# Kernel tuning notes

Measured on AMD Instinct MI355X. Metric: run time of the kernel, lower is better.

## Reference

```python
import jax, jax.numpy as jnp
import numpy as np

PI = 3.141592653589793
B, N, NUM_CLASSES = 512, 128, 10
Q_LAYERS = 3

# state layout: [B, Xc, Xa, Yc, Ya, F]  (Xc/Yc = condition (pooled) dims, Xa/Ya = active dims, F = feature dim = 2)

def _qft2d(s):
    # unitary QFT over both active spatial axes
    s = jnp.fft.fft(s, axis=2, norm="ortho")
    return jnp.fft.fft(s, axis=4, norm="ortho")

def _iqft2d(s):
    s = jnp.fft.ifft(s, axis=2, norm="ortho")
    return jnp.fft.ifft(s, axis=4, norm="ortho")

def _pool(s):
    # move the most significant active qubit of each axis into the condition register
    b, xc, xa, yc, ya, f = s.shape
    s = s.reshape(b, xc, 2, xa // 2, yc, 2, ya // 2, f)
    return s.reshape(b, xc * 2, xa // 2, yc * 2, ya // 2, f)

def _multiplex(s, coeffs):
    # coeffs: [cx, cy, Xa, Ya, 3] Pauli coefficients; applies exp(-i a.sigma) on the
    # feature qubit per Fourier mode, conditioned on the most recently pooled bit per axis.
    cx, cy = coeffs.shape[0], coeffs.shape[1]
    b, xc, xa, yc, ya, f = s.shape
    s = s.reshape(b, xc // cx, cx, xa, yc // cy, cy, ya, f)
    c = jnp.transpose(coeffs, (0, 2, 1, 3, 4))[None, None, :, :, None]  # [1,1,cx,Xa,1,cy,Ya,3]
    ax, ay, az = c[..., 0], c[..., 1], c[..., 2]
    r = jnp.sqrt(ax * ax + ay * ay + az * az + 1e-20)
    cr = jnp.cos(r)
    sn = jnp.sin(r) / r
    u00 = (cr - 1j * az * sn).astype(s.dtype)
    u01 = ((-1j * ax - ay) * sn).astype(s.dtype)
    u10 = ((-1j * ax + ay) * sn).astype(s.dtype)
    u11 = (cr + 1j * az * sn).astype(s.dtype)
    p0, p1 = s[..., 0], s[..., 1]
    out = jnp.stack([u00 * p0 + u01 * p1, u10 * p0 + u11 * p1], axis=-1)
    return out.reshape(b, xc, xa, yc, ya, f)

def _forward(images, mux0, mux1, mux2, W, b_):
    # FRQI encoder: theta in brightness_range (0, pi); feature qubit cos/sin amplitudes
    theta = PI * images
    amp = jnp.stack([jnp.cos(theta * 0.5), jnp.sin(theta * 0.5)], axis=-1) / images.shape[-1]
    state = amp.astype(jnp.complex64)[:, None, :, None, :, :]  # [B,1,N,1,N,2]
    muxes = (mux0, mux1, mux2)
    state = _qft2d(state)
    for li, coeffs in enumerate(muxes):
        state = _multiplex(state, coeffs)
        if li < len(muxes) - 1:
            # reduced Fourier junction == IQFT -> pool -> QFT
            state = _qft2d(_pool(_iqft2d(state)))
        else:
            state = _iqft2d(state)
    # marginal measurement over condition registers -> [B, Xa, Ya, F]
    prob = jnp.sum(jnp.abs(state) ** 2, axis=(1, 3))
    flat = prob.reshape(prob.shape[0], -1)
    return flat @ W.T + b_

def setup_inputs() -> dict:
    key = jax.random.key(0)
    ks = jax.random.split(key, 6)
    scale = 2.0 * PI
    images = jax.random.uniform(ks[0], (B, N, N), dtype=jnp.float32)
    mux0 = jax.random.uniform(ks[1], (1, 1, 128, 128, 3), dtype=jnp.float32) * scale
    mux1 = jax.random.uniform(ks[2], (2, 2, 64, 64, 3), dtype=jnp.float32) * scale
    mux2 = jax.random.uniform(ks[3], (2, 2, 32, 32, 3), dtype=jnp.float32) * scale
    W = jax.random.normal(ks[4], (NUM_CLASSES, 32 * 32 * 2), dtype=jnp.float32) * 0.02
    b_ = jnp.zeros((NUM_CLASSES,), dtype=jnp.float32)
    return {"images": images, "mux0": mux0, "mux1": mux1, "mux2": mux2, "W": W, "b_": b_}

def reference(images, mux0, mux1, mux2, W, b_):
    return _forward(images, mux0, mux1, mux2, W, b_)
```

## Files before the change

kernel.cpp:

```cpp
#include <hip/hip_runtime.h>
#include <math.h>


#define PI_F 3.14159265358979323846f
#define P_ 128

__device__ __forceinline__ float2 cmul(float2 a, float2 b) {
    return make_float2(a.x * b.x - a.y * b.y, a.x * b.y + a.y * b.x);
}
__device__ __forceinline__ float2 cadd(float2 a, float2 b) {
    return make_float2(a.x + b.x, a.y + b.y);
}
__device__ __forceinline__ float2 scl(float2 a, float s) {
    return make_float2(a.x * s, a.y * s);
}
__device__ __forceinline__ void bfly_dif(float2& u, float2& v, float2 w) {
    float tx = u.x - v.x, ty = u.y - v.y;
    u.x += v.x; u.y += v.y;
    v.x = tx * w.x - ty * w.y;
    v.y = tx * w.y + ty * w.x;
}
__device__ __forceinline__ void bfly_dif1(float2& u, float2& v) {
    float tx = u.x - v.x, ty = u.y - v.y;
    u.x += v.x; u.y += v.y;
    v.x = tx; v.y = ty;
}
__device__ __forceinline__ void bfly_dit(float2& u, float2& v, float2 w) {
    float tx = v.x * w.x + v.y * w.y, ty = v.y * w.x - v.x * w.y;
    v.x = u.x - tx; v.y = u.y - ty;
    u.x += tx; u.y += ty;
}
__device__ __forceinline__ void bfly_dit1(float2& u, float2& v) {
    float tx = v.x, ty = v.y;
    v.x = u.x - tx; v.y = u.y - ty;
    u.x += tx; u.y += ty;
}

constexpr int clog2(int v) { return v <= 1 ? 0 : 1 + clog2(v >> 1); }

__device__ __forceinline__ int pf(int L, int idx) {
    int m = ((idx & 32) ? 13 : 0) ^ ((idx & 64) ? 22 : 0);
    return L * P_ + (idx ^ m);
}

template <int N, int S>
__device__ __forceinline__ void oidx(int j, int i[4], int& o) {
    constexpr int TPS = N / 4;
    constexpr int LT = clog2(TPS);
    int s = j >> LT;
    int jj = j & (TPS - 1);
    o = jj & (S - 1);
    int base = s * N + ((jj & ~(S - 1)) << 2) + o;
    i[0] = base; i[1] = base + S; i[2] = base + 2 * S; i[3] = base + 3 * S;
}

template <int S>
__device__ __forceinline__ void dif_pair(float2 r[4], int o, const float2* tw) {
    bfly_dif(r[0], r[2], tw[o * (32 / S)]);
    bfly_dif(r[1], r[3], tw[(o + S) * (32 / S)]);
    float2 wc = tw[o * (64 / S)];
    bfly_dif(r[0], r[1], wc);
    bfly_dif(r[2], r[3], wc);
}
template <int S>
__device__ __forceinline__ void dit_pair(float2 r[4], int o, const float2* tw) {
    float2 wc = tw[o * (64 / S)];
    bfly_dit(r[0], r[1], wc);
    bfly_dit(r[2], r[3], wc);
    bfly_dit(r[0], r[2], tw[o * (32 / S)]);
    bfly_dit(r[1], r[3], tw[(o + S) * (32 / S)]);
}

__device__ __forceinline__ void stf(float* bx, float* by, int a, float2 v) {
    bx[a] = v.x; by[a] = v.y;
}
__device__ __forceinline__ float2 ldf(const float* bx, const float* by, int a) {
    return make_float2(bx[a], by[a]);
}

template <int NW, int SW, int NR, int SR>
__device__ __forceinline__ int xchg(float* bx, float* by, int L, int j,
                                    float2 r[4]) {
    int iw[4], ow;
    oidx<NW, SW>(j, iw, ow);
    stf(bx, by, pf(L, iw[0]), r[0]); stf(bx, by, pf(L, iw[1]), r[1]);
    stf(bx, by, pf(L, iw[2]), r[2]); stf(bx, by, pf(L, iw[3]), r[3]);
    __builtin_amdgcn_wave_barrier();
    int ir[4], orr;
    oidx<NR, SR>(j, ir, orr);
    r[0] = ldf(bx, by, pf(L, ir[0])); r[1] = ldf(bx, by, pf(L, ir[1]));
    r[2] = ldf(bx, by, pf(L, ir[2])); r[3] = ldf(bx, by, pf(L, ir[3]));
    __builtin_amdgcn_wave_barrier();
    return orr;
}

__device__ __forceinline__ void tw_init(float2* tw, int tid) {
    if (tid < 64) {
        float s, c;
        sincosf(-(2.0f * PI_F / 128.0f) * (float)tid, &s, &c);
        tw[tid] = make_float2(c, s);
    }
}

__global__ __launch_bounds__(256) void k0_prep(const float* __restrict__ mux0,
                                               const float* __restrict__ mux1,
                                               const float* __restrict__ mux2,
                                               float2* __restrict__ U0,
                                               float2* __restrict__ U1,
                                               float2* __restrict__ U2) {
    int t = blockIdx.x * 256 + threadIdx.x;
    const float* src;
    float2* dst;
    if (t < 16384) {
        int xb = t >> 7, yb = t & 127;
        int rx = __brev((unsigned)xb) >> 25;
        int ry = __brev((unsigned)yb) >> 25;
        src = mux0 + ((size_t)rx * 128 + ry) * 3;
        dst = U0 + (size_t)t * 4;
    } else if (t < 32768) {
        int u = t - 16384;
        int yam = u & 63, xam = (u >> 6) & 63, cy = (u >> 12) & 1, cx = (u >> 13) & 1;
        int rx = __brev((unsigned)xam) >> 26;
        int ry = __brev((unsigned)yam) >> 26;
        src = mux1 + ((size_t)(((cx * 2 + cy) * 64 + rx) * 64 + ry)) * 3;
        dst = U1 + (size_t)u * 4;
    } else if (t < 36864) {
        int u = t - 32768;
        int yam = u & 31, xam = (u >> 5) & 31, cy = (u >> 10) & 1, cx = (u >> 11) & 1;
        int rx = __brev((unsigned)xam) >> 27;
        int ry = __brev((unsigned)yam) >> 27;
        src = mux2 + ((size_t)(((cx * 2 + cy) * 32 + rx) * 32 + ry)) * 3;
        dst = U2 + (size_t)u * 4;
    } else {
        return;
    }
    float ax = src[0], ay = src[1], az = src[2];
    float r = sqrtf(ax * ax + ay * ay + az * az + 1e-20f);
    float cr = cosf(r);
    float snr = sinf(r) / r;
    dst[0] = make_float2(cr, -az * snr);
    dst[1] = make_float2(-ay * snr, -ax * snr);
    dst[2] = make_float2(ay * snr, -ax * snr);
    dst[3] = make_float2(cr, az * snr);
}

__global__ __launch_bounds__(256) void k1_encode(const float* __restrict__ img,
                                                 float2* __restrict__ S) {
    __shared__ float Ax[8 * P_], Ay[8 * P_], Bx[8 * P_], By[8 * P_];
    __shared__ float2 tw[64];
    int tid = threadIdx.x;
    tw_init(tw, tid);
    int b = blockIdx.x >> 5;
    int X0 = (blockIdx.x & 31) * 4;
    int L = tid >> 5, j = tid & 31;
    int row = L >> 1, f = L & 1;
    const float* ip = img + ((size_t)(b * 128) + X0 + row) * 128;
    float2 r[4];
#pragma unroll
    for (int q = 0; q < 4; ++q) {
        float v = ip[j + 32 * q];
        float s, c;
        sincosf(0.5f * PI_F * v, &s, &c);
        float a = f ? s : c;
        r[q] = make_float2(a * (1.0f / 128.0f), 0.0f);
    }
    __syncthreads();
    dif_pair<32>(r, j, tw);
    int o = xchg<128, 32, 128, 8>(Ax, Ay, L, j, r);
    dif_pair<8>(r, o, tw);
    o = xchg<128, 8, 128, 2>(Bx, By, L, j, r);
    dif_pair<2>(r, o, tw);
    o = xchg<128, 2, 128, 1>(Ax, Ay, L, j, r);
    bfly_dif1(r[0], r[1]); bfly_dif1(r[2], r[3]);
    float2* op = S + ((size_t)((b * 128 + X0 + row) * 2 + f)) * 128 + 4 * j;
    float4* gp = (float4*)op;
    gp[0] = make_float4(r[0].x, r[0].y, r[1].x, r[1].y);
    gp[1] = make_float4(r[2].x, r[2].y, r[3].x, r[3].y);
}

__global__ __launch_bounds__(256) void k2_col0(float2* __restrict__ S,
                                               const float2* __restrict__ U0) {
    __shared__ float Ax[8 * P_], Ay[8 * P_], Bx[8 * P_], By[8 * P_];
    __shared__ float2 tw[64];
    int tid = threadIdx.x;
    tw_init(tw, tid);
    int b = blockIdx.x >> 5;
    int s_ = blockIdx.x & 31;
    int Y0 = (((s_ & 7) << 2) | (s_ >> 3)) * 4;
    {
        int X = tid & 127, f = tid >> 7;
        const float4* gp = (const float4*)(S + ((size_t)((b * 128 + X) * 2 + f)) * 128 + Y0);
        float4 v0 = gp[0], v1 = gp[1];
        stf(Ax, Ay, pf(f * 4 + 0, X), make_float2(v0.x, v0.y));
        stf(Ax, Ay, pf(f * 4 + 1, X), make_float2(v0.z, v0.w));
        stf(Ax, Ay, pf(f * 4 + 2, X), make_float2(v1.x, v1.y));
        stf(Ax, Ay, pf(f * 4 + 3, X), make_float2(v1.z, v1.w));
    }
    __syncthreads();
    int L = tid >> 5, j = tid & 31;
    float2 r[4];
    int o;
    {
        int ir[4];
        oidx<128, 32>(j, ir, o);
        r[0] = ldf(Ax, Ay, pf(L, ir[0])); r[1] = ldf(Ax, Ay, pf(L, ir[1]));
        r[2] = ldf(Ax, Ay, pf(L, ir[2])); r[3] = ldf(Ax, Ay, pf(L, ir[3]));
    }
    dif_pair<32>(r, o, tw);
    o = xchg<128, 32, 128, 8>(Bx, By, L, j, r);
    dif_pair<8>(r, o, tw);
    o = xchg<128, 8, 128, 2>(Ax, Ay, L, j, r);
    dif_pair<2>(r, o, tw);
    {
        int iw[4], ow;
        oidx<128, 2>(j, iw, ow);
        stf(Bx, By, pf(L, iw[0]), r[0]); stf(Bx, By, pf(L, iw[1]), r[1]);
        stf(Bx, By, pf(L, iw[2]), r[2]); stf(Bx, By, pf(L, iw[3]), r[3]);
    }
    __syncthreads();
    int yl = tid >> 6, m2 = (tid & 63) * 2;
    r[0] = ldf(Bx, By, pf(yl, m2));     r[1] = ldf(Bx, By, pf(4 + yl, m2));
    r[2] = ldf(Bx, By, pf(yl, m2 + 1)); r[3] = ldf(Bx, By, pf(4 + yl, m2 + 1));
    bfly_dif1(r[0], r[2]); bfly_dif1(r[1], r[3]);
    {
        const float2* U = U0 + ((size_t)m2 * 128 + (Y0 + yl)) * 4;
        float2 p0 = r[0], p1 = r[1];
        r[0] = cadd(cmul(U[0], p0), cmul(U[1], p1));
        r[1] = cadd(cmul(U[2], p0), cmul(U[3], p1));
        U = U0 + ((size_t)(m2 + 1) * 128 + (Y0 + yl)) * 4;
        p0 = r[2]; p1 = r[3];
        r[2] = cadd(cmul(U[0], p0), cmul(U[1], p1));
        r[3] = cadd(cmul(U[2], p0), cmul(U[3], p1));
    }
    bfly_dit1(r[0], r[2]); bfly_dit1(r[1], r[3]);
    stf(Ax, Ay, pf(yl, m2), r[0]);     stf(Ax, Ay, pf(4 + yl, m2), r[1]);
    stf(Ax, Ay, pf(yl, m2 + 1), r[2]); stf(Ax, Ay, pf(4 + yl, m2 + 1), r[3]);
    __syncthreads();
    {
        int ir[4];
        oidx<128, 2>(j, ir, o);
        r[0] = ldf(Ax, Ay, pf(L, ir[0])); r[1] = ldf(Ax, Ay, pf(L, ir[1]));
        r[2] = ldf(Ax, Ay, pf(L, ir[2])); r[3] = ldf(Ax, Ay, pf(L, ir[3]));
    }
    dit_pair<2>(r, o, tw);
    o = xchg<128, 2, 128, 8>(Bx, By, L, j, r);
    dit_pair<8>(r, o, tw);
    o = xchg<128, 8, 128, 32>(Ax, Ay, L, j, r);
    dit_pair<32>(r, o, tw);
    {
        float2 w = tw[2 * o];
        bfly_dif(r[0], r[1], w); bfly_dif(r[2], r[3], w);
    }
    o = xchg<128, 32, 64, 8>(Bx, By, L, j, r);
    dif_pair<8>(r, o, tw);
    o = xchg<64, 8, 64, 2>(Ax, Ay, L, j, r);
    dif_pair<2>(r, o, tw);
    o = xchg<64, 2, 64, 1>(Bx, By, L, j, r);
    bfly_dif1(r[0], r[1]); bfly_dif1(r[2], r[3]);
    {
        int iw[4], ow;
        oidx<64, 1>(j, iw, ow);
        const float sc = 1.0f / 128.0f;
        stf(Ax, Ay, pf(L, iw[0]), scl(r[0], sc));
        stf(Ax, Ay, pf(L, iw[1]), scl(r[1], sc));
        stf(Ax, Ay, pf(L, iw[2]), scl(r[2], sc));
        stf(Ax, Ay, pf(L, iw[3]), scl(r[3], sc));
    }
    __syncthreads();
    {
        int X = tid & 127, f = tid >> 7;
        float2 e0 = ldf(Ax, Ay, pf(f * 4 + 0, X));
        float2 e1 = ldf(Ax, Ay, pf(f * 4 + 1, X));
        float2 e2 = ldf(Ax, Ay, pf(f * 4 + 2, X));
        float2 e3 = ldf(Ax, Ay, pf(f * 4 + 3, X));
        float4* gp = (float4*)(S + ((size_t)((b * 128 + X) * 2 + f)) * 128 + Y0);
        gp[0] = make_float4(e0.x, e0.y, e1.x, e1.y);
        gp[1] = make_float4(e2.x, e2.y, e3.x, e3.y);
    }
}

__global__ __launch_bounds__(256) void k3_row1(float2* __restrict__ S,
                                               const float2* __restrict__ U1) {
    __shared__ float Ax[8 * P_], Ay[8 * P_], Bx[8 * P_], By[8 * P_];
    __shared__ float2 tw[64];
    int tid = threadIdx.x;
    tw_init(tw, tid);
    int b = blockIdx.x >> 5;
    int X0 = (blockIdx.x & 31) * 4;
    int L = tid >> 5, j = tid & 31;
    int row = L >> 1, f = L & 1;
    float2* gl = S + ((size_t)((b * 128 + X0 + row) * 2 + f)) * 128;
    float2 r[4];
    {
        const float4* gp = (const float4*)(gl + 4 * j);
        float4 v0 = gp[0], v1 = gp[1];
        r[0] = make_float2(v0.x, v0.y); r[1] = make_float2(v0.z, v0.w);
        r[2] = make_float2(v1.x, v1.y); r[3] = make_float2(v1.z, v1.w);
    }
    __syncthreads();
    dit_pair<1>(r, 0, tw);
    int o = xchg<128, 1, 128, 4>(Ax, Ay, L, j, r);
    dit_pair<4>(r, o, tw);
    o = xchg<128, 4, 128, 16>(Bx, By, L, j, r);
    dit_pair<16>(r, o, tw);
    o = xchg<128, 16, 128, 32>(Ax, Ay, L, j, r);
    bfly_dit(r[0], r[2], tw[o]);
    bfly_dit(r[1], r[3], tw[o + 32]);
    {
        float2 w = tw[2 * o];
        bfly_dif(r[0], r[1], w); bfly_dif(r[2], r[3], w);
    }
    o = xchg<128, 32, 64, 8>(Bx, By, L, j, r);
    dif_pair<8>(r, o, tw);
    o = xchg<64, 8, 64, 2>(Ax, Ay, L, j, r);
    dif_pair<2>(r, o, tw);
    {
        int iw[4], ow;
        oidx<64, 2>(j, iw, ow);
        stf(Bx, By, pf(L, iw[0]), r[0]); stf(Bx, By, pf(L, iw[1]), r[1]);
        stf(Bx, By, pf(L, iw[2]), r[2]); stf(Bx, By, pf(L, iw[3]), r[3]);
    }
    __syncthreads();
    int row2 = tid >> 6, m2 = (tid & 63) * 2;
    r[0] = ldf(Bx, By, pf(row2 * 2, m2));
    r[1] = ldf(Bx, By, pf(row2 * 2 + 1, m2));
    r[2] = ldf(Bx, By, pf(row2 * 2, m2 + 1));
    r[3] = ldf(Bx, By, pf(row2 * 2 + 1, m2 + 1));
    bfly_dif1(r[0], r[2]); bfly_dif1(r[1], r[3]);
    {
        int X = X0 + row2;
        int cx = X >> 6, xam = X & 63;
        int cy0 = m2 >> 6, yam0 = m2 & 63;
        const float2* U =
            U1 + ((size_t)((((cx << 1) | cy0) << 6 | xam) << 6 | yam0)) * 4;
        float2 p0 = r[0], p1 = r[1];
        r[0] = cadd(cmul(U[0], p0), cmul(U[1], p1));
        r[1] = cadd(cmul(U[2], p0), cmul(U[3], p1));
        int cy1 = (m2 + 1) >> 6, yam1 = (m2 + 1) & 63;
        U = U1 + ((size_t)((((cx << 1) | cy1) << 6 | xam) << 6 | yam1)) * 4;
        p0 = r[2]; p1 = r[3];
        r[2] = cadd(cmul(U[0], p0), cmul(U[1], p1));
        r[3] = cadd(cmul(U[2], p0), cmul(U[3], p1));
    }
    bfly_dit1(r[0], r[2]); bfly_dit1(r[1], r[3]);
    stf(Ax, Ay, pf(row2 * 2, m2), r[0]);
    stf(Ax, Ay, pf(row2 * 2 + 1, m2), r[1]);
    stf(Ax, Ay, pf(row2 * 2, m2 + 1), r[2]);
    stf(Ax, Ay, pf(row2 * 2 + 1, m2 + 1), r[3]);
    __syncthreads();
    {
        int ir[4];
        oidx<64, 2>(j, ir, o);
        r[0] = ldf(Ax, Ay, pf(L, ir[0])); r[1] = ldf(Ax, Ay, pf(L, ir[1]));
        r[2] = ldf(Ax, Ay, pf(L, ir[2])); r[3] = ldf(Ax, Ay, pf(L, ir[3]));
    }
    dit_pair<2>(r, o, tw);
    o = xchg<64, 2, 64, 8>(Bx, By, L, j, r);
    dit_pair<8>(r, o, tw);
    o = xchg<64, 8, 64, 16>(Ax, Ay, L, j, r);
    bfly_dit(r[0], r[2], tw[2 * o]);
    bfly_dit(r[1], r[3], tw[2 * o + 32]);
    {
        float2 w = tw[4 * o];
        bfly_dif(r[0], r[1], w); bfly_dif(r[2], r[3], w);
    }
    o = xchg<64, 16, 32, 4>(Bx, By, L, j, r);
    dif_pair<4>(r, o, tw);
    o = xchg<32, 4, 32, 1>(Ax, Ay, L, j, r);
    dif_pair<1>(r, 0, tw);
    {
        int iw[4], ow;
        oidx<32, 1>(j, iw, ow);
        const float sc = 1.0f / 8192.0f;
        float4* gp = (float4*)(gl + iw[0]);
        gp[0] = make_float4(r[0].x * sc, r[0].y * sc, r[1].x * sc, r[1].y * sc);
        gp[1] = make_float4(r[2].x * sc, r[2].y * sc, r[3].x * sc, r[3].y * sc);
    }
}

__global__ __launch_bounds__(256) void k4_col2(float2* __restrict__ S,
                                               const float2* __restrict__ U2) {
    __shared__ float Ax[8 * P_], Ay[8 * P_], Bx[8 * P_], By[8 * P_];
    __shared__ float2 tw[64];
    int tid = threadIdx.x;
    tw_init(tw, tid);
    int b = blockIdx.x >> 5;
    int s_ = blockIdx.x & 31;
    int Y0 = (((s_ & 7) << 2) | (s_ >> 3)) * 4;
    {
        int X = tid & 127, f = tid >> 7;
        const float4* gp = (const float4*)(S + ((size_t)((b * 128 + X) * 2 + f)) * 128 + Y0);
        float4 v0 = gp[0], v1 = gp[1];
        stf(Ax, Ay, pf(f * 4 + 0, X), make_float2(v0.x, v0.y));
        stf(Ax, Ay, pf(f * 4 + 1, X), make_float2(v0.z, v0.w));
        stf(Ax, Ay, pf(f * 4 + 2, X), make_float2(v1.x, v1.y));
        stf(Ax, Ay, pf(f * 4 + 3, X), make_float2(v1.z, v1.w));
    }
    __syncthreads();
    int L = tid >> 5, j = tid & 31;
    float2 r[4];
    int o;
    {
        int ir[4];
        oidx<64, 1>(j, ir, o);
        r[0] = ldf(Ax, Ay, pf(L, ir[0])); r[1] = ldf(Ax, Ay, pf(L, ir[1]));
        r[2] = ldf(Ax, Ay, pf(L, ir[2])); r[3] = ldf(Ax, Ay, pf(L, ir[3]));
    }
    dit_pair<1>(r, 0, tw);
    o = xchg<64, 1, 64, 4>(Bx, By, L, j, r);
    dit_pair<4>(r, o, tw);
    o = xchg<64, 4, 64, 16>(Ax, Ay, L, j, r);
    dit_pair<16>(r, o, tw);
    {
        float2 w = tw[4 * o];
        bfly_dif(r[0], r[1], w); bfly_dif(r[2], r[3], w);
    }
    o = xchg<64, 16, 32, 4>(Bx, By, L, j, r);
    dif_pair<4>(r, o, tw);
    o = xchg<32, 4, 32, 1>(Ax, Ay, L, j, r);
    dif_pair<1>(r, 0, tw);
    {
        int iw[4], ow;
        oidx<32, 1>(j, iw, ow);
        stf(Bx, By, pf(L, iw[0]), r[0]); stf(Bx, By, pf(L, iw[1]), r[1]);
        stf(Bx, By, pf(L, iw[2]), r[2]); stf(Bx, By, pf(L, iw[3]), r[3]);
    }
    __syncthreads();
    int yl = tid >> 6, m2 = (tid & 63) * 2;
    r[0] = ldf(Bx, By, pf(yl, m2));     r[1] = ldf(Bx, By, pf(4 + yl, m2));
    r[2] = ldf(Bx, By, pf(yl, m2 + 1)); r[3] = ldf(Bx, By, pf(4 + yl, m2 + 1));
    {
        int Ym = Y0 + yl;
        int cy = (Ym >> 5) & 1, yam = Ym & 31;
        int cx = (m2 >> 5) & 1, xam = m2 & 31;
        const float2* U =
            U2 + ((size_t)((((cx << 1) | cy) << 5 | xam) << 5 | yam)) * 4;
        float2 p0 = r[0], p1 = r[1];
        r[0] = cadd(cmul(U[0], p0), cmul(U[1], p1));
        r[1] = cadd(cmul(U[2], p0), cmul(U[3], p1));
        int X1 = m2 + 1;
        cx = (X1 >> 5) & 1; xam = X1 & 31;
        U = U2 + ((size_t)((((cx << 1) | cy) << 5 | xam) << 5 | yam)) * 4;
        p0 = r[2]; p1 = r[3];
        r[2] = cadd(cmul(U[0], p0), cmul(U[1], p1));
        r[3] = cadd(cmul(U[2], p0), cmul(U[3], p1));
    }
    bfly_dit1(r[0], r[2]); bfly_dit1(r[1], r[3]);
    stf(Ax, Ay, pf(yl, m2), r[0]);     stf(Ax, Ay, pf(4 + yl, m2), r[1]);
    stf(Ax, Ay, pf(yl, m2 + 1), r[2]); stf(Ax, Ay, pf(4 + yl, m2 + 1), r[3]);
    __syncthreads();
    {
        int ir[4];
        oidx<32, 2>(j, ir, o);
        r[0] = ldf(Ax, Ay, pf(L, ir[0])); r[1] = ldf(Ax, Ay, pf(L, ir[1]));
        r[2] = ldf(Ax, Ay, pf(L, ir[2])); r[3] = ldf(Ax, Ay, pf(L, ir[3]));
    }
    dit_pair<2>(r, o, tw);
    o = xchg<32, 2, 32, 8>(Bx, By, L, j, r);
    dit_pair<8>(r, o, tw);
    {
        int iw[4], ow;
        oidx<32, 8>(j, iw, ow);
        const float sc = 1.0f / 2048.0f;
        stf(Ax, Ay, pf(L, iw[0]), scl(r[0], sc));
        stf(Ax, Ay, pf(L, iw[1]), scl(r[1], sc));
        stf(Ax, Ay, pf(L, iw[2]), scl(r[2], sc));
        stf(Ax, Ay, pf(L, iw[3]), scl(r[3], sc));
    }
    __syncthreads();
    {
        int X = tid & 127, f = tid >> 7;
        float2 e0 = ldf(Ax, Ay, pf(f * 4 + 0, X));
        float2 e1 = ldf(Ax, Ay, pf(f * 4 + 1, X));
        float2 e2 = ldf(Ax, Ay, pf(f * 4 + 2, X));
        float2 e3 = ldf(Ax, Ay, pf(f * 4 + 3, X));
        float4* gp = (float4*)(S + ((size_t)((b * 128 + X) * 2 + f)) * 128 + Y0);
        gp[0] = make_float4(e0.x, e0.y, e1.x, e1.y);
        gp[1] = make_float4(e2.x, e2.y, e3.x, e3.y);
    }
}

__global__ __launch_bounds__(256) void k5_prob(const float2* __restrict__ S,
                                               float* __restrict__ prob) {
    __shared__ float Ax[8 * P_], Ay[8 * P_], Bx[8 * P_], By[8 * P_];
    __shared__ float2 tw[64];
    int tid = threadIdx.x;
    tw_init(tw, tid);
    int b = blockIdx.x >> 5;
    int xa = blockIdx.x & 31;
    int L = tid >> 5, j = tid & 31;
    int row = L >> 1, f = L & 1;
    const float2* gl = S + ((size_t)((b * 128 + xa + 32 * row) * 2 + f)) * 128;
    float2 r[4];
    int o;
    int i0[4];
    oidx<32, 1>(j, i0, o);
    {
        const float4* gp = (const float4*)(gl + i0[0]);
        float4 v0 = gp[0], v1 = gp[1];
        r[0] = make_float2(v0.x, v0.y); r[1] = make_float2(v0.z, v0.w);
        r[2] = make_float2(v1.x, v1.y); r[3] = make_float2(v1.z, v1.w);
    }
    __syncthreads();
    dit_pair<1>(r, 0, tw);
    o = xchg<32, 1, 32, 4>(Ax, Ay, L, j, r);
    dit_pair<4>(r, o, tw);
    o = xchg<32, 4, 32, 8>(Bx, By, L, j, r);
    bfly_dit(r[0], r[2], tw[4 * o]);
    bfly_dit(r[1], r[3], tw[4 * o + 32]);
    {
        int iw[4], ow;
        oidx<32, 8>(j, iw, ow);
        stf(Ax, Ay, pf(L, iw[0]), r[0]); stf(Ax, Ay, pf(L, iw[1]), r[1]);
        stf(Ax, Ay, pf(L, iw[2]), r[2]); stf(Ax, Ay, pf(L, iw[3]), r[3]);
    }
    __syncthreads();
    if (tid < 64) {
        int ya = tid >> 1, ff = tid & 1;
        float s = 0.0f;
        for (int rr = 0; rr < 4; ++rr)
            for (int yc = 0; yc < 4; ++yc) {
                float2 v = ldf(Ax, Ay, pf(rr * 2 + ff, yc * 32 + ya));
                s += v.x * v.x + v.y * v.y;
            }
        prob[((size_t)(b * 32 + xa) * 32 + ya) * 2 + ff] = s * (1.0f / 1024.0f);
    }
}

__global__ __launch_bounds__(256) void k6_linear(const float* __restrict__ prob,
                                                 const float* __restrict__ W,
                                                 const float* __restrict__ bv,
                                                 float* __restrict__ out) {
    __shared__ float red[40];
    int b = blockIdx.x;
    int tid = threadIdx.x;
    float acc[10];
#pragma unroll
    for (int c = 0; c < 10; ++c) acc[c] = 0.0f;
    for (int j = tid; j < 2048; j += 256) {
        float p = prob[(size_t)b * 2048 + j];
#pragma unroll
        for (int c = 0; c < 10; ++c) acc[c] += p * W[c * 2048 + j];
    }
    int wv = tid >> 6, ln = tid & 63;
#pragma unroll
    for (int c = 0; c < 10; ++c) {
        float s = acc[c];
        for (int off = 32; off > 0; off >>= 1) s += __shfl_down(s, off);
        if (ln == 0) red[wv * 10 + c] = s;
    }
    __syncthreads();
    if (tid < 10)
        out[b * 10 + tid] =
            red[tid] + red[10 + tid] + red[20 + tid] + red[30 + tid] + bv[tid];
}

extern "C" void kernel_launch(void* const* d_in, const int* in_sizes, int n_in,
                              void* d_out, int out_size, void* d_ws,
                              size_t ws_size, hipStream_t stream) {
    const float* images = (const float*)d_in[0];
    const float* mux0 = (const float*)d_in[1];
    const float* mux1 = (const float*)d_in[2];
    const float* mux2 = (const float*)d_in[3];
    const float* W = (const float*)d_in[4];
    const float* bv = (const float*)d_in[5];
    float* out = (float*)d_out;

    float2* ws0 = (float2*)d_ws;
    const size_t STATE_F2 = (size_t)512 * 128 * 128 * 2;
    float2* S = ws0;
    float2* U0 = ws0 + STATE_F2;
    float2* U1 = U0 + 65536;
    float2* U2 = U1 + 65536;
    float* prob = (float*)(U2 + 16384);
    const size_t needed =
        (STATE_F2 + 65536 + 65536 + 16384) * sizeof(float2) +
        (size_t)512 * 2048 * sizeof(float);
    if (ws_size < needed) return;

    k0_prep<<<144, 256, 0, stream>>>(mux0, mux1, mux2, U0, U1, U2);
    k1_encode<<<16384, 256, 0, stream>>>(images, S);
    k2_col0<<<16384, 256, 0, stream>>>(S, U0);
    k3_row1<<<16384, 256, 0, stream>>>(S, U1);
    k4_col2<<<16384, 256, 0, stream>>>(S, U2);
    k5_prob<<<16384, 256, 0, stream>>>(S, prob);
    k6_linear<<<512, 256, 0, stream>>>(prob, W, bv, out);
}
```

Measured before the change: 398.6 us.

## Fuse encode, all FFT/multiplex stages and measurement into one per-image kernel

Replaces the five per-stage kernels, which each read and write the full complex state in global memory, with a single kernel that keeps one whole 128x128x2 image state in registers plus a 64KB LDS tile, using 1024 threads per block. Axis switches are done with in-LDS transposes, and the U0/U2 coefficient tables are relaid out in the prep kernel to match the new access order. This removes roughly 256MB of global state traffic per stage. The cost is heavy register pressure (32 complex values per thread), only 512 blocks in the grid, and many block-wide syncs.

```diff
diff --git a/kernel.cpp b/kernel.cpp
--- a/kernel.cpp
+++ b/kernel.cpp
@@ -78,28 +78,129 @@
     return make_float2(bx[a], by[a]);
 }
 
+__device__ __forceinline__ void xch8(float* Xp, float* Yp, int g,
+                                     const int* iw, const int* ir,
+                                     float2 (&r)[8][4]) {
+    const int la = 2 * g, lb = 2 * g + 1;
+#pragma unroll
+    for (int m = 0; m < 4; ++m) {
+#pragma unroll
+        for (int q = 0; q < 4; ++q) {
+            stf(Xp, Yp, pf(la, iw[q]), r[m][q]);
+            stf(Xp, Yp, pf(lb, iw[q]), r[m + 4][q]);
+        }
+        __builtin_amdgcn_wave_barrier();
+#pragma unroll
+        for (int q = 0; q < 4; ++q) {
+            r[m][q]     = ldf(Xp, Yp, pf(la, ir[q]));
+            r[m + 4][q] = ldf(Xp, Yp, pf(lb, ir[q]));
+        }
+        __builtin_amdgcn_wave_barrier();
+    }
+}
+
 template <int NW, int SW, int NR, int SR>
-__device__ __forceinline__ int xchg(float* bx, float* by, int L, int j,
-                                    float2 r[4]) {
-    int iw[4], ow;
+__device__ __forceinline__ int XC(float* Xp, float* Yp, int g, int j,
+                                  float2 (&r)[8][4]) {
+    int iw[4], ow, ir[4], orr;
     oidx<NW, SW>(j, iw, ow);
-    stf(bx, by, pf(L, iw[0]), r[0]); stf(bx, by, pf(L, iw[1]), r[1]);
-    stf(bx, by, pf(L, iw[2]), r[2]); stf(bx, by, pf(L, iw[3]), r[3]);
-    __builtin_amdgcn_wave_barrier();
-    int ir[4], orr;
     oidx<NR, SR>(j, ir, orr);
-    r[0] = ldf(bx, by, pf(L, ir[0])); r[1] = ldf(bx, by, pf(L, ir[1]));
-    r[2] = ldf(bx, by, pf(L, ir[2])); r[3] = ldf(bx, by, pf(L, ir[3]));
-    __builtin_amdgcn_wave_barrier();
+    (void)ow;
+    xch8(Xp, Yp, g, iw, ir, r);
     return orr;
 }
 
-__device__ __forceinline__ void tw_init(float2* tw, int tid) {
-    if (tid < 64) {
-        float s, c;
-        sincosf(-(2.0f * PI_F / 128.0f) * (float)tid, &s, &c);
-        tw[tid] = make_float2(c, s);
-    }
+__device__ __forceinline__ void xpose44(float2 (&r)[8][4]) {
+#pragma unroll
+    for (int f0 = 0; f0 < 8; f0 += 4)
+#pragma unroll
+        for (int a = 0; a < 4; ++a)
+#pragma unroll
+            for (int bq = a + 1; bq < 4; ++bq) {
+                float2 t = r[f0 + a][bq];
+                r[f0 + a][bq] = r[f0 + bq][a];
+                r[f0 + bq][a] = t;
+            }
+}
+
+__device__ __forceinline__ void mkF(int j, int* i) {
+    i[0] = 2 * j; i[1] = 2 * j + 1; i[2] = 64 + 2 * j; i[3] = 65 + 2 * j;
+}
+__device__ __forceinline__ void mkF4(int j, int* i) {
+    int b = (j >> 4) * 32 + (j & 15);
+    i[0] = b; i[1] = b + 16; i[2] = b + 64; i[3] = b + 80;
+}
+
+__device__ __forceinline__ void muxop(const float2* __restrict__ U,
+                                      float2& a, float2& b) {
+    float2 p0 = a, p1 = b;
+    a = cadd(cmul(U[0], p0), cmul(U[1], p1));
+    b = cadd(cmul(U[2], p0), cmul(U[3], p1));
+}
+
+template <int MODE>
+__device__ __forceinline__ void tposeA(float* Xp, float* Yp, int g, int j,
+                                       const int* is, float2 (&r)[8][4]) {
+#pragma unroll
+    for (int c = 0; c < 4; ++c) {
+        const int fc = c >> 1, h = c & 1;
+        __syncthreads();
+#pragma unroll
+        for (int e = 0; e < 2; ++e) {
+            const int k = fc * 4 + 2 * h + e;
+            const int Xl = g + 32 * e;
+#pragma unroll
+            for (int q = 0; q < 4; ++q) {
+                int a = Xl * P_ + ((is[q] + Xl) & 127);
+                Xp[a] = r[k][q].x; Yp[a] = r[k][q].y;
+            }
+        }
+        __syncthreads();
+#pragma unroll
+        for (int e = 0; e < 2; ++e) {
+            const int Xl = (MODE == 0) ? (j + 32 * e) : (2 * j + e);
+#pragma unroll
+            for (int d = 0; d < 4; ++d) {
+                int a = Xl * P_ + ((g + 32 * d + Xl) & 127);
+                r[fc * 4 + 2 * h + e][d] = make_float2(Xp[a], Yp[a]);
+            }
+        }
+    }
+    __syncthreads();
+    xpose44(r);
+}
+
+__device__ __forceinline__ void tposeB(float* Xp, float* Yp, int g, int j,
+                                       const int* is, const int* id,
+                                       float2 (&r)[8][4]) {
+    xpose44(r);
+#pragma unroll
+    for (int c = 0; c < 4; ++c) {
+        const int fc = c >> 1, h = c & 1;
+        __syncthreads();
+#pragma unroll
+        for (int e = 0; e < 2; ++e) {
+            const int q = 2 * h + e;
+            const int Xl = is[q] & 63;
+#pragma unroll
+            for (int d = 0; d < 4; ++d) {
+                int a = Xl * P_ + ((g + 32 * d + Xl) & 127);
+                float2 v = r[fc * 4 + q][d];
+                Xp[a] = v.x; Yp[a] = v.y;
+            }
+        }
+        __syncthreads();
+#pragma unroll
+        for (int e = 0; e < 2; ++e) {
+            const int Xl = g + 32 * e;
+#pragma unroll
+            for (int qy = 0; qy < 4; ++qy) {
+                int a = Xl * P_ + ((id[qy] + Xl) & 127);
+                r[fc * 4 + 2 * h + e][qy] = make_float2(Xp[a], Yp[a]);
+            }
+        }
+    }
+    __syncthreads();
 }
 
 __global__ __launch_bounds__(256) void k0_prep(const float* __restrict__ mux0,
@@ -116,7 +217,7 @@
         int rx = __brev((unsigned)xb) >> 25;
         int ry = __brev((unsigned)yb) >> 25;
         src = mux0 + ((size_t)rx * 128 + ry) * 3;
-        dst = U0 + (size_t)t * 4;
+        dst = U0 + ((size_t)yb * 128 + xb) * 4;
     } else if (t < 32768) {
         int u = t - 16384;
         int yam = u & 63, xam = (u >> 6) & 63, cy = (u >> 12) & 1, cx = (u >> 13) & 1;
@@ -130,7 +231,7 @@
         int rx = __brev((unsigned)xam) >> 27;
         int ry = __brev((unsigned)yam) >> 27;
         src = mux2 + ((size_t)(((cx * 2 + cy) * 32 + rx) * 32 + ry)) * 3;
-        dst = U2 + (size_t)u * 4;
+        dst = U2 + ((size_t)(((yam * 2 + cx) * 2 + cy) * 32 + xam)) * 4;
     } else {
         return;
     }
@@ -144,386 +245,280 @@
     dst[3] = make_float2(cr, az * snr);
 }
 
-__global__ __launch_bounds__(256) void k1_encode(const float* __restrict__ img,
-                                                 float2* __restrict__ S) {
-    __shared__ float Ax[8 * P_], Ay[8 * P_], Bx[8 * P_], By[8 * P_];
-    __shared__ float2 tw[64];
-    int tid = threadIdx.x;
-    tw_init(tw, tid);
-    int b = blockIdx.x >> 5;
-    int X0 = (blockIdx.x & 31) * 4;
-    int L = tid >> 5, j = tid & 31;
-    int row = L >> 1, f = L & 1;
-    const float* ip = img + ((size_t)(b * 128) + X0 + row) * 128;
-    float2 r[4];
-#pragma unroll
-    for (int q = 0; q < 4; ++q) {
-        float v = ip[j + 32 * q];
+__global__ __launch_bounds__(1024, 4) void kfuse(const float* __restrict__ img,
+                                                 const float2* __restrict__ U0,
+                                                 const float2* __restrict__ U1,
+                                                 const float2* __restrict__ U2,
+                                                 float* __restrict__ prob) {
+    extern __shared__ float smem[];
+    float* Xp = smem;
+    float* Yp = smem + 8192;
+    float2* tw = (float2*)(smem + 16384);
+
+    const int tid = threadIdx.x;
+    const int b = blockIdx.x;
+    const int g = tid >> 5;
+    const int j = tid & 31;
+
+    if (tid < 64) {
         float s, c;
-        sincosf(0.5f * PI_F * v, &s, &c);
-        float a = f ? s : c;
-        r[q] = make_float2(a * (1.0f / 128.0f), 0.0f);
+        sincosf(-(2.0f * PI_F / 128.0f) * (float)tid, &s, &c);
+        tw[tid] = make_float2(c, s);
+    }
+
+    float2 r[8][4];
+    int o;
+
+    {
+        const float* ib = img + (size_t)b * 16384;
+#pragma unroll
+        for (int k = 0; k < 4; ++k) {
+            const float* ip = ib + (g + 32 * k) * 128;
+#pragma unroll
+            for (int q = 0; q < 4; ++q) {
+                float v = ip[j + 32 * q];
+                float s, c;
+                sincosf(0.5f * PI_F * v, &s, &c);
+                r[k][q]     = make_float2(c * (1.0f / 128.0f), 0.0f);
+                r[k + 4][q] = make_float2(s * (1.0f / 128.0f), 0.0f);
+            }
+        }
     }
     __syncthreads();
-    dif_pair<32>(r, j, tw);
-    int o = xchg<128, 32, 128, 8>(Ax, Ay, L, j, r);
-    dif_pair<8>(r, o, tw);
-    o = xchg<128, 8, 128, 2>(Bx, By, L, j, r);
-    dif_pair<2>(r, o, tw);
-    o = xchg<128, 2, 128, 1>(Ax, Ay, L, j, r);
-    bfly_dif1(r[0], r[1]); bfly_dif1(r[2], r[3]);
-    float2* op = S + ((size_t)((b * 128 + X0 + row) * 2 + f)) * 128 + 4 * j;
-    float4* gp = (float4*)op;
-    gp[0] = make_float4(r[0].x, r[0].y, r[1].x, r[1].y);
-    gp[1] = make_float4(r[2].x, r[2].y, r[3].x, r[3].y);
-}
-
-__global__ __launch_bounds__(256) void k2_col0(float2* __restrict__ S,
-                                               const float2* __restrict__ U0) {
-    __shared__ float Ax[8 * P_], Ay[8 * P_], Bx[8 * P_], By[8 * P_];
-    __shared__ float2 tw[64];
-    int tid = threadIdx.x;
-    tw_init(tw, tid);
-    int b = blockIdx.x >> 5;
-    int s_ = blockIdx.x & 31;
-    int Y0 = (((s_ & 7) << 2) | (s_ >> 3)) * 4;
-    {
-        int X = tid & 127, f = tid >> 7;
-        const float4* gp = (const float4*)(S + ((size_t)((b * 128 + X) * 2 + f)) * 128 + Y0);
-        float4 v0 = gp[0], v1 = gp[1];
-        stf(Ax, Ay, pf(f * 4 + 0, X), make_float2(v0.x, v0.y));
-        stf(Ax, Ay, pf(f * 4 + 1, X), make_float2(v0.z, v0.w));
-        stf(Ax, Ay, pf(f * 4 + 2, X), make_float2(v1.x, v1.y));
-        stf(Ax, Ay, pf(f * 4 + 3, X), make_float2(v1.z, v1.w));
-    }
-    __syncthreads();
-    int L = tid >> 5, j = tid & 31;
-    float2 r[4];
-    int o;
-    {
-        int ir[4];
-        oidx<128, 32>(j, ir, o);
-        r[0] = ldf(Ax, Ay, pf(L, ir[0])); r[1] = ldf(Ax, Ay, pf(L, ir[1]));
-        r[2] = ldf(Ax, Ay, pf(L, ir[2])); r[3] = ldf(Ax, Ay, pf(L, ir[3]));
-    }
-    dif_pair<32>(r, o, tw);
-    o = xchg<128, 32, 128, 8>(Bx, By, L, j, r);
-    dif_pair<8>(r, o, tw);
-    o = xchg<128, 8, 128, 2>(Ax, Ay, L, j, r);
-    dif_pair<2>(r, o, tw);
-    {
-        int iw[4], ow;
-        oidx<128, 2>(j, iw, ow);
-        stf(Bx, By, pf(L, iw[0]), r[0]); stf(Bx, By, pf(L, iw[1]), r[1]);
-        stf(Bx, By, pf(L, iw[2]), r[2]); stf(Bx, By, pf(L, iw[3]), r[3]);
-    }
-    __syncthreads();
-    int yl = tid >> 6, m2 = (tid & 63) * 2;
-    r[0] = ldf(Bx, By, pf(yl, m2));     r[1] = ldf(Bx, By, pf(4 + yl, m2));
-    r[2] = ldf(Bx, By, pf(yl, m2 + 1)); r[3] = ldf(Bx, By, pf(4 + yl, m2 + 1));
-    bfly_dif1(r[0], r[2]); bfly_dif1(r[1], r[3]);
-    {
-        const float2* U = U0 + ((size_t)m2 * 128 + (Y0 + yl)) * 4;
-        float2 p0 = r[0], p1 = r[1];
-        r[0] = cadd(cmul(U[0], p0), cmul(U[1], p1));
-        r[1] = cadd(cmul(U[2], p0), cmul(U[3], p1));
-        U = U0 + ((size_t)(m2 + 1) * 128 + (Y0 + yl)) * 4;
-        p0 = r[2]; p1 = r[3];
-        r[2] = cadd(cmul(U[0], p0), cmul(U[1], p1));
-        r[3] = cadd(cmul(U[2], p0), cmul(U[3], p1));
-    }
-    bfly_dit1(r[0], r[2]); bfly_dit1(r[1], r[3]);
-    stf(Ax, Ay, pf(yl, m2), r[0]);     stf(Ax, Ay, pf(4 + yl, m2), r[1]);
-    stf(Ax, Ay, pf(yl, m2 + 1), r[2]); stf(Ax, Ay, pf(4 + yl, m2 + 1), r[3]);
-    __syncthreads();
-    {
-        int ir[4];
-        oidx<128, 2>(j, ir, o);
-        r[0] = ldf(Ax, Ay, pf(L, ir[0])); r[1] = ldf(Ax, Ay, pf(L, ir[1]));
-        r[2] = ldf(Ax, Ay, pf(L, ir[2])); r[3] = ldf(Ax, Ay, pf(L, ir[3]));
-    }
-    dit_pair<2>(r, o, tw);
-    o = xchg<128, 2, 128, 8>(Bx, By, L, j, r);
-    dit_pair<8>(r, o, tw);
-    o = xchg<128, 8, 128, 32>(Ax, Ay, L, j, r);
-    dit_pair<32>(r, o, tw);
-    {
-        float2 w = tw[2 * o];
-        bfly_dif(r[0], r[1], w); bfly_dif(r[2], r[3], w);
-    }
-    o = xchg<128, 32, 64, 8>(Bx, By, L, j, r);
-    dif_pair<8>(r, o, tw);
-    o = xchg<64, 8, 64, 2>(Ax, Ay, L, j, r);
-    dif_pair<2>(r, o, tw);
-    o = xchg<64, 2, 64, 1>(Bx, By, L, j, r);
-    bfly_dif1(r[0], r[1]); bfly_dif1(r[2], r[3]);
-    {
-        int iw[4], ow;
-        oidx<64, 1>(j, iw, ow);
+#pragma unroll
+    for (int k = 0; k < 8; ++k) dif_pair<32>(r[k], j, tw);
+    o = XC<128, 32, 128, 8>(Xp, Yp, g, j, r);
+#pragma unroll
+    for (int k = 0; k < 8; ++k) dif_pair<8>(r[k], o, tw);
+    o = XC<128, 8, 128, 2>(Xp, Yp, g, j, r);
+#pragma unroll
+    for (int k = 0; k < 8; ++k) dif_pair<2>(r[k], o, tw);
+    o = XC<128, 2, 128, 1>(Xp, Yp, g, j, r);
+#pragma unroll
+    for (int k = 0; k < 8; ++k) { bfly_dif1(r[k][0], r[k][1]); bfly_dif1(r[k][2], r[k][3]); }
+
+    {
+        int is[4] = {4 * j, 4 * j + 1, 4 * j + 2, 4 * j + 3};
+        tposeA<0>(Xp, Yp, g, j, is, r);
+    }
+
+#pragma unroll
+    for (int k = 0; k < 8; ++k) dif_pair<32>(r[k], j, tw);
+    o = XC<128, 32, 128, 8>(Xp, Yp, g, j, r);
+#pragma unroll
+    for (int k = 0; k < 8; ++k) dif_pair<8>(r[k], o, tw);
+    o = XC<128, 8, 128, 2>(Xp, Yp, g, j, r);
+#pragma unroll
+    for (int k = 0; k < 8; ++k) dif_pair<2>(r[k], o, tw);
+    o = XC<128, 2, 128, 1>(Xp, Yp, g, j, r);
+#pragma unroll
+    for (int k = 0; k < 8; ++k) { bfly_dif1(r[k][0], r[k][1]); bfly_dif1(r[k][2], r[k][3]); }
+#pragma unroll
+    for (int k = 0; k < 4; ++k) {
+        const float2* Ub = U0 + ((size_t)(g + 32 * k) * 128 + 4 * j) * 4;
+#pragma unroll
+        for (int q = 0; q < 4; ++q) muxop(Ub + (size_t)q * 4, r[k][q], r[k + 4][q]);
+    }
+#pragma unroll
+    for (int k = 0; k < 8; ++k) dit_pair<1>(r[k], 0, tw);
+    o = XC<128, 1, 128, 4>(Xp, Yp, g, j, r);
+#pragma unroll
+    for (int k = 0; k < 8; ++k) dit_pair<4>(r[k], o, tw);
+    o = XC<128, 4, 128, 16>(Xp, Yp, g, j, r);
+#pragma unroll
+    for (int k = 0; k < 8; ++k) dit_pair<16>(r[k], o, tw);
+    o = XC<128, 16, 128, 32>(Xp, Yp, g, j, r);
+#pragma unroll
+    for (int k = 0; k < 8; ++k) { bfly_dit(r[k][0], r[k][2], tw[o]); bfly_dit(r[k][1], r[k][3], tw[o + 32]); }
+#pragma unroll
+    for (int k = 0; k < 8; ++k) { float2 w = tw[2 * o]; bfly_dif(r[k][0], r[k][1], w); bfly_dif(r[k][2], r[k][3], w); }
+    o = XC<128, 32, 64, 8>(Xp, Yp, g, j, r);
+#pragma unroll
+    for (int k = 0; k < 8; ++k) dif_pair<8>(r[k], o, tw);
+    o = XC<64, 8, 64, 2>(Xp, Yp, g, j, r);
+#pragma unroll
+    for (int k = 0; k < 8; ++k) dif_pair<2>(r[k], o, tw);
+    {
+        int iw_[4], o_, ir_[4];
+        oidx<64, 2>(j, iw_, o_);
+        mkF(j, ir_);
+        xch8(Xp, Yp, g, iw_, ir_, r);
+    }
+#pragma unroll
+    for (int k = 0; k < 8; ++k) {
+        bfly_dif1(r[k][0], r[k][1]); bfly_dif1(r[k][2], r[k][3]);
         const float sc = 1.0f / 128.0f;
-        stf(Ax, Ay, pf(L, iw[0]), scl(r[0], sc));
-        stf(Ax, Ay, pf(L, iw[1]), scl(r[1], sc));
-        stf(Ax, Ay, pf(L, iw[2]), scl(r[2], sc));
-        stf(Ax, Ay, pf(L, iw[3]), scl(r[3], sc));
-    }
-    __syncthreads();
-    {
-        int X = tid & 127, f = tid >> 7;
-        float2 e0 = ldf(Ax, Ay, pf(f * 4 + 0, X));
-        float2 e1 = ldf(Ax, Ay, pf(f * 4 + 1, X));
-        float2 e2 = ldf(Ax, Ay, pf(f * 4 + 2, X));
-        float2 e3 = ldf(Ax, Ay, pf(f * 4 + 3, X));
-        float4* gp = (float4*)(S + ((size_t)((b * 128 + X) * 2 + f)) * 128 + Y0);
-        gp[0] = make_float4(e0.x, e0.y, e1.x, e1.y);
-        gp[1] = make_float4(e2.x, e2.y, e3.x, e3.y);
-    }
-}
-
-__global__ __launch_bounds__(256) void k3_row1(float2* __restrict__ S,
-                                               const float2* __restrict__ U1) {
-    __shared__ float Ax[8 * P_], Ay[8 * P_], Bx[8 * P_], By[8 * P_];
-    __shared__ float2 tw[64];
-    int tid = threadIdx.x;
-    tw_init(tw, tid);
-    int b = blockIdx.x >> 5;
-    int X0 = (blockIdx.x & 31) * 4;
-    int L = tid >> 5, j = tid & 31;
-    int row = L >> 1, f = L & 1;
-    float2* gl = S + ((size_t)((b * 128 + X0 + row) * 2 + f)) * 128;
-    float2 r[4];
-    {
-        const float4* gp = (const float4*)(gl + 4 * j);
-        float4 v0 = gp[0], v1 = gp[1];
-        r[0] = make_float2(v0.x, v0.y); r[1] = make_float2(v0.z, v0.w);
-        r[2] = make_float2(v1.x, v1.y); r[3] = make_float2(v1.z, v1.w);
-    }
-    __syncthreads();
-    dit_pair<1>(r, 0, tw);
-    int o = xchg<128, 1, 128, 4>(Ax, Ay, L, j, r);
-    dit_pair<4>(r, o, tw);
-    o = xchg<128, 4, 128, 16>(Bx, By, L, j, r);
-    dit_pair<16>(r, o, tw);
-    o = xchg<128, 16, 128, 32>(Ax, Ay, L, j, r);
-    bfly_dit(r[0], r[2], tw[o]);
-    bfly_dit(r[1], r[3], tw[o + 32]);
-    {
-        float2 w = tw[2 * o];
-        bfly_dif(r[0], r[1], w); bfly_dif(r[2], r[3], w);
-    }
-    o = xchg<128, 32, 64, 8>(Bx, By, L, j, r);
-    dif_pair<8>(r, o, tw);
-    o = xchg<64, 8, 64, 2>(Ax, Ay, L, j, r);
-    dif_pair<2>(r, o, tw);
-    {
-        int iw[4], ow;
-        oidx<64, 2>(j, iw, ow);
-        stf(Bx, By, pf(L, iw[0]), r[0]); stf(Bx, By, pf(L, iw[1]), r[1]);
-        stf(Bx, By, pf(L, iw[2]), r[2]); stf(Bx, By, pf(L, iw[3]), r[3]);
-    }
-    __syncthreads();
-    int row2 = tid >> 6, m2 = (tid & 63) * 2;
-    r[0] = ldf(Bx, By, pf(row2 * 2, m2));
-    r[1] = ldf(Bx, By, pf(row2 * 2 + 1, m2));
-    r[2] = ldf(Bx, By, pf(row2 * 2, m2 + 1));
-    r[3] = ldf(Bx, By, pf(row2 * 2 + 1, m2 + 1));
-    bfly_dif1(r[0], r[2]); bfly_dif1(r[1], r[3]);
-    {
-        int X = X0 + row2;
-        int cx = X >> 6, xam = X & 63;
-        int cy0 = m2 >> 6, yam0 = m2 & 63;
-        const float2* U =
-            U1 + ((size_t)((((cx << 1) | cy0) << 6 | xam) << 6 | yam0)) * 4;
-        float2 p0 = r[0], p1 = r[1];
-        r[0] = cadd(cmul(U[0], p0), cmul(U[1], p1));
-        r[1] = cadd(cmul(U[2], p0), cmul(U[3], p1));
-        int cy1 = (m2 + 1) >> 6, yam1 = (m2 + 1) & 63;
-        U = U1 + ((size_t)((((cx << 1) | cy1) << 6 | xam) << 6 | yam1)) * 4;
-        p0 = r[2]; p1 = r[3];
-        r[2] = cadd(cmul(U[0], p0), cmul(U[1], p1));
-        r[3] = cadd(cmul(U[2], p0), cmul(U[3], p1));
-    }
-    bfly_dit1(r[0], r[2]); bfly_dit1(r[1], r[3]);
-    stf(Ax, Ay, pf(row2 * 2, m2), r[0]);
-    stf(Ax, Ay, pf(row2 * 2 + 1, m2), r[1]);
-    stf(Ax, Ay, pf(row2 * 2, m2 + 1), r[2]);
-    stf(Ax, Ay, pf(row2 * 2 + 1, m2 + 1), r[3]);
-    __syncthreads();
-    {
-        int ir[4];
-        oidx<64, 2>(j, ir, o);
-        r[0] = ldf(Ax, Ay, pf(L, ir[0])); r[1] = ldf(Ax, Ay, pf(L, ir[1]));
-        r[2] = ldf(Ax, Ay, pf(L, ir[2])); r[3] = ldf(Ax, Ay, pf(L, ir[3]));
-    }
-    dit_pair<2>(r, o, tw);
-    o = xchg<64, 2, 64, 8>(Bx, By, L, j, r);
-    dit_pair<8>(r, o, tw);
-    o = xchg<64, 8, 64, 16>(Ax, Ay, L, j, r);
-    bfly_dit(r[0], r[2], tw[2 * o]);
-    bfly_dit(r[1], r[3], tw[2 * o + 32]);
-    {
-        float2 w = tw[4 * o];
-        bfly_dif(r[0], r[1], w); bfly_dif(r[2], r[3], w);
-    }
-    o = xchg<64, 16, 32, 4>(Bx, By, L, j, r);
-    dif_pair<4>(r, o, tw);
-    o = xchg<32, 4, 32, 1>(Ax, Ay, L, j, r);
-    dif_pair<1>(r, 0, tw);
-    {
-        int iw[4], ow;
-        oidx<32, 1>(j, iw, ow);
+#pragma unroll
+        for (int q = 0; q < 4; ++q) r[k][q] = scl(r[k][q], sc);
+    }
+
+    {
+        int is[4], id[4];
+        mkF(j, is);
+        id[0] = 4 * j; id[1] = 4 * j + 1; id[2] = 4 * j + 2; id[3] = 4 * j + 3;
+        tposeB(Xp, Yp, g, j, is, id, r);
+    }
+
+#pragma unroll
+    for (int k = 0; k < 8; ++k) dit_pair<1>(r[k], 0, tw);
+    o = XC<128, 1, 128, 4>(Xp, Yp, g, j, r);
+#pragma unroll
+    for (int k = 0; k < 8; ++k) dit_pair<4>(r[k], o, tw);
+    o = XC<128, 4, 128, 16>(Xp, Yp, g, j, r);
+#pragma unroll
+    for (int k = 0; k < 8; ++k) dit_pair<16>(r[k], o, tw);
+    o = XC<128, 16, 128, 32>(Xp, Yp, g, j, r);
+#pragma unroll
+    for (int k = 0; k < 8; ++k) { bfly_dit(r[k][0], r[k][2], tw[o]); bfly_dit(r[k][1], r[k][3], tw[o + 32]); }
+#pragma unroll
+    for (int k = 0; k < 8; ++k) { float2 w = tw[2 * o]; bfly_dif(r[k][0], r[k][1], w); bfly_dif(r[k][2], r[k][3], w); }
+    o = XC<128, 32, 64, 8>(Xp, Yp, g, j, r);
+#pragma unroll
+    for (int k = 0; k < 8; ++k) dif_pair<8>(r[k], o, tw);
+    o = XC<64, 8, 64, 2>(Xp, Yp, g, j, r);
+#pragma unroll
+    for (int k = 0; k < 8; ++k) dif_pair<2>(r[k], o, tw);
+    o = XC<64, 2, 64, 1>(Xp, Yp, g, j, r);
+#pragma unroll
+    for (int k = 0; k < 8; ++k) { bfly_dif1(r[k][0], r[k][1]); bfly_dif1(r[k][2], r[k][3]); }
+    {
+        const int s = j >> 4, jj = j & 15;
+#pragma unroll
+        for (int k = 0; k < 4; ++k) {
+            const int cx = k >> 1;
+            const int xam = g + 32 * (k & 1);
+            const float2* Ub =
+                U1 + ((size_t)((((((cx << 1) | s) << 6) | xam) << 6) | (4 * jj))) * 4;
+#pragma unroll
+            for (int q = 0; q < 4; ++q) muxop(Ub + (size_t)q * 4, r[k][q], r[k + 4][q]);
+        }
+    }
+#pragma unroll
+    for (int k = 0; k < 8; ++k) dit_pair<1>(r[k], 0, tw);
+    o = XC<64, 1, 64, 4>(Xp, Yp, g, j, r);
+#pragma unroll
+    for (int k = 0; k < 8; ++k) dit_pair<4>(r[k], o, tw);
+    o = XC<64, 4, 64, 16>(Xp, Yp, g, j, r);
+#pragma unroll
+    for (int k = 0; k < 8; ++k) dit_pair<16>(r[k], o, tw);
+#pragma unroll
+    for (int k = 0; k < 8; ++k) { float2 w = tw[4 * o]; bfly_dif(r[k][0], r[k][1], w); bfly_dif(r[k][2], r[k][3], w); }
+    o = XC<64, 16, 32, 4>(Xp, Yp, g, j, r);
+#pragma unroll
+    for (int k = 0; k < 8; ++k) dif_pair<4>(r[k], o, tw);
+    o = XC<32, 4, 32, 1>(Xp, Yp, g, j, r);
+#pragma unroll
+    for (int k = 0; k < 8; ++k) {
+        dif_pair<1>(r[k], 0, tw);
         const float sc = 1.0f / 8192.0f;
-        float4* gp = (float4*)(gl + iw[0]);
-        gp[0] = make_float4(r[0].x * sc, r[0].y * sc, r[1].x * sc, r[1].y * sc);
-        gp[1] = make_float4(r[2].x * sc, r[2].y * sc, r[3].x * sc, r[3].y * sc);
-    }
-}
-
-__global__ __launch_bounds__(256) void k4_col2(float2* __restrict__ S,
-                                               const float2* __restrict__ U2) {
-    __shared__ float Ax[8 * P_], Ay[8 * P_], Bx[8 * P_], By[8 * P_];
-    __shared__ float2 tw[64];
-    int tid = threadIdx.x;
-    tw_init(tw, tid);
-    int b = blockIdx.x >> 5;
-    int s_ = blockIdx.x & 31;
-    int Y0 = (((s_ & 7) << 2) | (s_ >> 3)) * 4;
-    {
-        int X = tid & 127, f = tid >> 7;
-        const float4* gp = (const float4*)(S + ((size_t)((b * 128 + X) * 2 + f)) * 128 + Y0);
-        float4 v0 = gp[0], v1 = gp[1];
-        stf(Ax, Ay, pf(f * 4 + 0, X), make_float2(v0.x, v0.y));
-        stf(Ax, Ay, pf(f * 4 + 1, X), make_float2(v0.z, v0.w));
-        stf(Ax, Ay, pf(f * 4 + 2, X), make_float2(v1.x, v1.y));
-        stf(Ax, Ay, pf(f * 4 + 3, X), make_float2(v1.z, v1.w));
-    }
-    __syncthreads();
-    int L = tid >> 5, j = tid & 31;
-    float2 r[4];
-    int o;
-    {
-        int ir[4];
-        oidx<64, 1>(j, ir, o);
-        r[0] = ldf(Ax, Ay, pf(L, ir[0])); r[1] = ldf(Ax, Ay, pf(L, ir[1]));
-        r[2] = ldf(Ax, Ay, pf(L, ir[2])); r[3] = ldf(Ax, Ay, pf(L, ir[3]));
-    }
-    dit_pair<1>(r, 0, tw);
-    o = xchg<64, 1, 64, 4>(Bx, By, L, j, r);
-    dit_pair<4>(r, o, tw);
-    o = xchg<64, 4, 64, 16>(Ax, Ay, L, j, r);
-    dit_pair<16>(r, o, tw);
-    {
-        float2 w = tw[4 * o];
-        bfly_dif(r[0], r[1], w); bfly_dif(r[2], r[3], w);
-    }
-    o = xchg<64, 16, 32, 4>(Bx, By, L, j, r);
-    dif_pair<4>(r, o, tw);
-    o = xchg<32, 4, 32, 1>(Ax, Ay, L, j, r);
-    dif_pair<1>(r, 0, tw);
-    {
-        int iw[4], ow;
-        oidx<32, 1>(j, iw, ow);
-        stf(Bx, By, pf(L, iw[0]), r[0]); stf(Bx, By, pf(L, iw[1]), r[1]);
-        stf(Bx, By, pf(L, iw[2]), r[2]); stf(Bx, By, pf(L, iw[3]), r[3]);
-    }
-    __syncthreads();
-    int yl = tid >> 6, m2 = (tid & 63) * 2;
-    r[0] = ldf(Bx, By, pf(yl, m2));     r[1] = ldf(Bx, By, pf(4 + yl, m2));
-    r[2] = ldf(Bx, By, pf(yl, m2 + 1)); r[3] = ldf(Bx, By, pf(4 + yl, m2 + 1));
-    {
-        int Ym = Y0 + yl;
-        int cy = (Ym >> 5) & 1, yam = Ym & 31;
-        int cx = (m2 >> 5) & 1, xam = m2 & 31;
-        const float2* U =
-            U2 + ((size_t)((((cx << 1) | cy) << 5 | xam) << 5 | yam)) * 4;
-        float2 p0 = r[0], p1 = r[1];
-        r[0] = cadd(cmul(U[0], p0), cmul(U[1], p1));
-        r[1] = cadd(cmul(U[2], p0), cmul(U[3], p1));
-        int X1 = m2 + 1;
-        cx = (X1 >> 5) & 1; xam = X1 & 31;
-        U = U2 + ((size_t)((((cx << 1) | cy) << 5 | xam) << 5 | yam)) * 4;
-        p0 = r[2]; p1 = r[3];
-        r[2] = cadd(cmul(U[0], p0), cmul(U[1], p1));
-        r[3] = cadd(cmul(U[2], p0), cmul(U[3], p1));
-    }
-    bfly_dit1(r[0], r[2]); bfly_dit1(r[1], r[3]);
-    stf(Ax, Ay, pf(yl, m2), r[0]);     stf(Ax, Ay, pf(4 + yl, m2), r[1]);
-    stf(Ax, Ay, pf(yl, m2 + 1), r[2]); stf(Ax, Ay, pf(4 + yl, m2 + 1), r[3]);
-    __syncthreads();
-    {
-        int ir[4];
-        oidx<32, 2>(j, ir, o);
-        r[0] = ldf(Ax, Ay, pf(L, ir[0])); r[1] = ldf(Ax, Ay, pf(L, ir[1]));
-        r[2] = ldf(Ax, Ay, pf(L, ir[2])); r[3] = ldf(Ax, Ay, pf(L, ir[3]));
-    }
-    dit_pair<2>(r, o, tw);
-    o = xchg<32, 2, 32, 8>(Bx, By, L, j, r);
-    dit_pair<8>(r, o, tw);
-    {
-        int iw[4], ow;
-        oidx<32, 8>(j, iw, ow);
-        const float sc = 1.0f / 2048.0f;
-        stf(Ax, Ay, pf(L, iw[0]), scl(r[0], sc));
-        stf(Ax, Ay, pf(L, iw[1]), scl(r[1], sc));
-        stf(Ax, Ay, pf(L, iw[2]), scl(r[2], sc));
-        stf(Ax, Ay, pf(L, iw[3]), scl(r[3], sc));
-    }
-    __syncthreads();
-    {
-        int X = tid & 127, f = tid >> 7;
-        float2 e0 = ldf(Ax, Ay, pf(f * 4 + 0, X));
-        float2 e1 = ldf(Ax, Ay, pf(f * 4 + 1, X));
-        float2 e2 = ldf(Ax, Ay, pf(f * 4 + 2, X));
-        float2 e3 = ldf(Ax, Ay, pf(f * 4 + 3, X));
-        float4* gp = (float4*)(S + ((size_t)((b * 128 + X) * 2 + f)) * 128 + Y0);
-        gp[0] = make_float4(e0.x, e0.y, e1.x, e1.y);
-        gp[1] = make_float4(e2.x, e2.y, e3.x, e3.y);
-    }
-}
-
-__global__ __launch_bounds__(256) void k5_prob(const float2* __restrict__ S,
-                                               float* __restrict__ prob) {
-    __shared__ float Ax[8 * P_], Ay[8 * P_], Bx[8 * P_], By[8 * P_];
-    __shared__ float2 tw[64];
-    int tid = threadIdx.x;
-    tw_init(tw, tid);
-    int b = blockIdx.x >> 5;
-    int xa = blockIdx.x & 31;
-    int L = tid >> 5, j = tid & 31;
-    int row = L >> 1, f = L & 1;
-    const float2* gl = S + ((size_t)((b * 128 + xa + 32 * row) * 2 + f)) * 128;
-    float2 r[4];
-    int o;
-    int i0[4];
-    oidx<32, 1>(j, i0, o);
-    {
-        const float4* gp = (const float4*)(gl + i0[0]);
-        float4 v0 = gp[0], v1 = gp[1];
-        r[0] = make_float2(v0.x, v0.y); r[1] = make_float2(v0.z, v0.w);
-        r[2] = make_float2(v1.x, v1.y); r[3] = make_float2(v1.z, v1.w);
-    }
-    __syncthreads();
-    dit_pair<1>(r, 0, tw);
-    o = xchg<32, 1, 32, 4>(Ax, Ay, L, j, r);
-    dit_pair<4>(r, o, tw);
-    o = xchg<32, 4, 32, 8>(Bx, By, L, j, r);
-    bfly_dit(r[0], r[2], tw[4 * o]);
-    bfly_dit(r[1], r[3], tw[4 * o + 32]);
-    {
-        int iw[4], ow;
-        oidx<32, 8>(j, iw, ow);
-        stf(Ax, Ay, pf(L, iw[0]), r[0]); stf(Ax, Ay, pf(L, iw[1]), r[1]);
-        stf(Ax, Ay, pf(L, iw[2]), r[2]); stf(Ax, Ay, pf(L, iw[3]), r[3]);
-    }
-    __syncthreads();
-    if (tid < 64) {
-        int ya = tid >> 1, ff = tid & 1;
-        float s = 0.0f;
-        for (int rr = 0; rr < 4; ++rr)
-            for (int yc = 0; yc < 4; ++yc) {
-                float2 v = ldf(Ax, Ay, pf(rr * 2 + ff, yc * 32 + ya));
-                s += v.x * v.x + v.y * v.y;
-            }
-        prob[((size_t)(b * 32 + xa) * 32 + ya) * 2 + ff] = s * (1.0f / 1024.0f);
+#pragma unroll
+        for (int q = 0; q < 4; ++q) r[k][q] = scl(r[k][q], sc);
+    }
+
+    {
+        int is[4], o_;
+        oidx<32, 1>(j, is, o_);
+        tposeA<1>(Xp, Yp, g, j, is, r);
+    }
+
+#pragma unroll
+    for (int k = 0; k < 8; ++k) { bfly_dit1(r[k][0], r[k][1]); bfly_dit1(r[k][2], r[k][3]); }
+    {
+        int iw_[4], ir_[4], o_;
+        mkF(j, iw_);
+        oidx<64, 2>(j, ir_, o_);
+        xch8(Xp, Yp, g, iw_, ir_, r);
+        o = o_;
+    }
+#pragma unroll
+    for (int k = 0; k < 8; ++k) dit_pair<2>(r[k], o, tw);
+    o = XC<64, 2, 64, 8>(Xp, Yp, g, j, r);
+#pragma unroll
+    for (int k = 0; k < 8; ++k) dit_pair<8>(r[k], o, tw);
+    o = XC<64, 8, 64, 16>(Xp, Yp, g, j, r);
+#pragma unroll
+    for (int k = 0; k < 8; ++k) { bfly_dit(r[k][0], r[k][2], tw[2 * o]); bfly_dit(r[k][1], r[k][3], tw[2 * (o + 16)]); }
+#pragma unroll
+    for (int k = 0; k < 8; ++k) { float2 w = tw[4 * o]; bfly_dif(r[k][0], r[k][1], w); bfly_dif(r[k][2], r[k][3], w); }
+    o = XC<64, 16, 32, 4>(Xp, Yp, g, j, r);
+#pragma unroll
+    for (int k = 0; k < 8; ++k) dif_pair<4>(r[k], o, tw);
+    o = XC<32, 4, 32, 1>(Xp, Yp, g, j, r);
+#pragma unroll
+    for (int k = 0; k < 8; ++k) dif_pair<1>(r[k], 0, tw);
+    {
+        const int s4 = j >> 3, jj8 = j & 7;
+#pragma unroll
+        for (int k = 0; k < 4; ++k) {
+            const float2* Ub =
+                U2 + ((size_t)((((g << 2) | ((s4 & 1) << 1) | (k & 1)) << 5) | (4 * jj8))) * 4;
+#pragma unroll
+            for (int q = 0; q < 4; ++q) muxop(Ub + (size_t)q * 4, r[k][q], r[k + 4][q]);
+        }
+    }
+#pragma unroll
+    for (int k = 0; k < 8; ++k) dit_pair<1>(r[k], 0, tw);
+    o = XC<32, 1, 32, 4>(Xp, Yp, g, j, r);
+#pragma unroll
+    for (int k = 0; k < 8; ++k) dit_pair<4>(r[k], o, tw);
+    {
+        int iw_[4], o_, ir_[4];
+        oidx<32, 4>(j, iw_, o_);
+        mkF4(j, ir_);
+        xch8(Xp, Yp, g, iw_, ir_, r);
+    }
+    {
+        const int m = j & 15;
+#pragma unroll
+        for (int k = 0; k < 8; ++k) {
+            float2 w = tw[4 * m];
+            bfly_dit(r[k][0], r[k][1], w);
+            bfly_dit(r[k][2], r[k][3], w);
+            const float sc = 1.0f / 2048.0f;
+#pragma unroll
+            for (int q = 0; q < 4; ++q) r[k][q] = scl(r[k][q], sc);
+        }
+    }
+
+    {
+        int is[4], id[4], o_;
+        mkF4(j, is);
+        oidx<32, 1>(j, id, o_);
+        tposeB(Xp, Yp, g, j, is, id, r);
+    }
+
+#pragma unroll
+    for (int k = 0; k < 8; ++k) dit_pair<1>(r[k], 0, tw);
+    o = XC<32, 1, 32, 4>(Xp, Yp, g, j, r);
+#pragma unroll
+    for (int k = 0; k < 8; ++k) dit_pair<4>(r[k], o, tw);
+    o = XC<32, 4, 32, 8>(Xp, Yp, g, j, r);
+#pragma unroll
+    for (int k = 0; k < 8; ++k) { bfly_dit(r[k][0], r[k][2], tw[4 * o]); bfly_dit(r[k][1], r[k][3], tw[4 * o + 32]); }
+    {
+        float p2[2][4];
+#pragma unroll
+        for (int f = 0; f < 2; ++f)
+#pragma unroll
+            for (int q = 0; q < 4; ++q) {
+                float s = 0.0f;
+#pragma unroll
+                for (int d = 0; d < 4; ++d) {
+                    float2 v = r[f * 4 + d][q];
+                    s += v.x * v.x + v.y * v.y;
+                }
+                s += __shfl_xor(s, 8);
+                s += __shfl_xor(s, 16);
+                p2[f][q] = s;
+            }
+        if ((j >> 3) == 0) {
+            const int jj = j & 7;
+            float2* pp = (float2*)(prob + (size_t)(b * 32 + g) * 64);
+#pragma unroll
+            for (int q = 0; q < 4; ++q)
+                pp[jj + 8 * q] = make_float2(p2[0][q] * (1.0f / 1024.0f),
+                                             p2[1][q] * (1.0f / 1024.0f));
+        }
     }
 }
 
@@ -566,23 +561,18 @@
     const float* bv = (const float*)d_in[5];
     float* out = (float*)d_out;
 
-    float2* ws0 = (float2*)d_ws;
-    const size_t STATE_F2 = (size_t)512 * 128 * 128 * 2;
-    float2* S = ws0;
-    float2* U0 = ws0 + STATE_F2;
+    float2* U0 = (float2*)d_ws;
     float2* U1 = U0 + 65536;
     float2* U2 = U1 + 65536;
     float* prob = (float*)(U2 + 16384);
     const size_t needed =
-        (STATE_F2 + 65536 + 65536 + 16384) * sizeof(float2) +
+        (size_t)(65536 + 65536 + 16384) * sizeof(float2) +
         (size_t)512 * 2048 * sizeof(float);
     if (ws_size < needed) return;
 
+    const int LDS_BYTES = (16384 + 128) * 4;
+
     k0_prep<<<144, 256, 0, stream>>>(mux0, mux1, mux2, U0, U1, U2);
-    k1_encode<<<16384, 256, 0, stream>>>(images, S);
-    k2_col0<<<16384, 256, 0, stream>>>(S, U0);
-    k3_row1<<<16384, 256, 0, stream>>>(S, U1);
-    k4_col2<<<16384, 256, 0, stream>>>(S, U2);
-    k5_prob<<<16384, 256, 0, stream>>>(S, prob);
+    kfuse<<<512, 1024, LDS_BYTES, stream>>>(images, U0, U1, U2, prob);
     k6_linear<<<512, 256, 0, stream>>>(prob, W, bv, out);
 }
```

New measurement: 350.0 us. 1.14x faster.
